# Performance work log

Measured on AMD Instinct MI355X. Metric: run time of the kernel, lower is better.

Reference implementation:

```python
import jax, jax.numpy as jnp
import numpy as np

N = 50000
E = 800000
IN_DIM = 256
HID = 32
HEADS = 4
OUT_DIM = 40
NEG_SLOPE = 0.2


def gat_layer(x, src, dst, W, a_src, a_dst, b, n_nodes, heads, ch, concat):
    # x: [N, F_in], W: [F_in, heads*ch], a_src/a_dst: [heads, ch], b: [out]
    h = (x @ W).reshape(n_nodes, heads, ch)                 # [N,H,C]
    alpha_s = jnp.einsum('nhc,hc->nh', h, a_src)            # [N,H]
    alpha_d = jnp.einsum('nhc,hc->nh', h, a_dst)            # [N,H]
    e = jax.nn.leaky_relu(alpha_s[src] + alpha_d[dst], NEG_SLOPE)  # [E,H]
    # segment softmax over destination neighborhoods (self-loops guarantee nonempty)
    m = jax.ops.segment_max(e, dst, num_segments=n_nodes)   # [N,H]
    e = jnp.exp(e - m[dst])
    denom = jax.ops.segment_sum(e, dst, num_segments=n_nodes)
    alpha = e / (denom[dst] + 1e-16)                         # [E,H]
    msg = h[src] * alpha[:, :, None]                         # [E,H,C]
    out = jax.ops.segment_sum(msg, dst, num_segments=n_nodes)  # [N,H,C]
    out = out.reshape(n_nodes, heads * ch) if concat else out.mean(axis=1)
    return out + b


def setup_inputs() -> dict:
    key = jax.random.key(0)
    ks = jax.random.split(key, 10)
    x = jax.random.normal(ks[0], (N, IN_DIM), dtype=jnp.float32)
    edge_index = jax.random.randint(ks[1], (2, E), 0, N, dtype=jnp.int32)
    s1 = 1.0 / np.sqrt(IN_DIM)
    s2 = 1.0 / np.sqrt(HID * HEADS)
    return {
        'x': x,
        'edge_index': edge_index,
        'W1': jax.random.normal(ks[2], (IN_DIM, HEADS * HID), dtype=jnp.float32) * s1,
        'a_src1': jax.random.normal(ks[3], (HEADS, HID), dtype=jnp.float32) * s1,
        'a_dst1': jax.random.normal(ks[4], (HEADS, HID), dtype=jnp.float32) * s1,
        'b1': jnp.zeros((HEADS * HID,), dtype=jnp.float32),
        'W2': jax.random.normal(ks[5], (HEADS * HID, OUT_DIM), dtype=jnp.float32) * s2,
        'a_src2': jax.random.normal(ks[6], (1, OUT_DIM), dtype=jnp.float32) * s2,
        'a_dst2': jax.random.normal(ks[7], (1, OUT_DIM), dtype=jnp.float32) * s2,
        'b2': jnp.zeros((OUT_DIM,), dtype=jnp.float32),
    }


def reference(x, edge_index, W1, a_src1, a_dst1, b1, W2, a_src2, a_dst2, b2):
    # PyG GATConv adds self-loops by default
    loops = jnp.arange(N, dtype=edge_index.dtype)
    src = jnp.concatenate([edge_index[0], loops])
    dst = jnp.concatenate([edge_index[1], loops])
    h = gat_layer(x, src, dst, W1, a_src1, a_dst1, b1, N, HEADS, HID, True)
    h = jax.nn.relu(h)
    out = gat_layer(h, src, dst, W2, a_src2, a_dst2, b2, N, 1, OUT_DIM, False)
    return jax.nn.log_softmax(out, axis=1)
```

## Files before the change

### kernel.cpp

```cpp
#include <hip/hip_runtime.h>
#include <math.h>

#define N_NODES 50000
#define N_EDGES 800000
#define IN_DIM  256
#define F1      128
#define HEADS   4
#define OUT_DIM 40
#define NEG     0.2f

#define NB   391
#define CAP  3072
#define EB   4096
#define PREW 16
#define G1B  782

typedef __attribute__((ext_vector_type(8))) short short8;
typedef __attribute__((ext_vector_type(4))) float float4v;

__device__ __forceinline__ unsigned short f2bf(float f) {
  unsigned int u = __float_as_uint(f);
  u += 0x7FFF + ((u >> 16) & 1);
  return (unsigned short)(u >> 16);
}
__device__ __forceinline__ float bf2f(unsigned short h) {
  return __uint_as_float((unsigned int)h << 16);
}
__device__ __forceinline__ float bflo(unsigned int u) { return __uint_as_float(u << 16); }
__device__ __forceinline__ float bfhi(unsigned int u) { return __uint_as_float(u & 0xffff0000u); }

__device__ __forceinline__ float lrelu(float e) { return e > 0.f ? e : e * NEG; }

__device__ __forceinline__ void gload_lds16(const void* g, void* l) {
  __builtin_amdgcn_global_load_lds(
      (const __attribute__((address_space(1))) unsigned int*)g,
      (__attribute__((address_space(3))) unsigned int*)l, 16, 0, 0);
}

__global__ __launch_bounds__(256) void pre_kernel(const float* __restrict__ W1,
                                                  unsigned short* __restrict__ wHi,
                                                  unsigned short* __restrict__ wLo,
                                                  const int* __restrict__ ei,
                                                  int* __restrict__ gcnt,
                                                  int2* __restrict__ gbucket) {
  __shared__ int smem[EB * 2 + NB * 3];
  if (blockIdx.x < PREW) {
    int tid = blockIdx.x * 256 + threadIdx.x;
    int kk = tid >> 9;
    int rest = tid & 511;
    int t = rest >> 6;
    int lane = rest & 63;
    int q = lane >> 4;
    int ln = lane & 15;
    int n = t * 16 + ln;
    unsigned int hi[4], lo[4];
#pragma unroll
    for (int jj = 0; jj < 4; jj++) {
      unsigned short h0, h1, l0, l1;
      {
        float v = W1[(kk * 32 + q * 8 + jj * 2) * F1 + n];
        h0 = f2bf(v); l0 = f2bf(v - bf2f(h0));
      }
      {
        float v = W1[(kk * 32 + q * 8 + jj * 2 + 1) * F1 + n];
        h1 = f2bf(v); l1 = f2bf(v - bf2f(h1));
      }
      hi[jj] = (unsigned int)h0 | ((unsigned int)h1 << 16);
      lo[jj] = (unsigned int)l0 | ((unsigned int)l1 << 16);
    }
    size_t base = (size_t)tid * 8;
    *(uint4*)&wHi[base] = make_uint4(hi[0], hi[1], hi[2], hi[3]);
    *(uint4*)&wLo[base] = make_uint4(lo[0], lo[1], lo[2], lo[3]);
  } else {
    int* ls = smem;
    int* ld = smem + EB;
    int* lcnt = smem + 2 * EB;
    int* lcur = lcnt + NB;
    int* gbaseS = lcur + NB;
    int tid = threadIdx.x;
    size_t base = (size_t)(blockIdx.x - PREW) * EB;
    for (int t = tid; t < NB; t += 256) { lcnt[t] = 0; lcur[t] = 0; }
    __syncthreads();
#pragma unroll
    for (int l = 0; l < EB / 256; l++) {
      int li = l * 256 + tid;
      size_t idx = base + li;
      int s = 0, d = -1;
      if (idx < N_EDGES) {
        s = ei[idx];
        d = ei[N_EDGES + idx];
        atomicAdd(&lcnt[d >> 7], 1);
      }
      ls[li] = s;
      ld[li] = d;
    }
    __syncthreads();
    for (int t = tid; t < NB; t += 256) gbaseS[t] = atomicAdd(&gcnt[t], lcnt[t]);
    __syncthreads();
#pragma unroll
    for (int l = 0; l < EB / 256; l++) {
      int li = l * 256 + tid;
      int d = ld[li];
      if (d >= 0) {
        int b = d >> 7;
        int r = gbaseS[b] + atomicAdd(&lcur[b], 1);
        if (r >= CAP) r = CAP - 1;
        gbucket[(size_t)b * CAP + r] = make_int2(ls[li], d);
      }
    }
  }
}

__global__ __launch_bounds__(256) void mid_kernel(
    const float* __restrict__ x, const unsigned short* __restrict__ wHi,
    const unsigned short* __restrict__ wLo,
    const float* __restrict__ a_src, const float* __restrict__ a_dst,
    unsigned short* __restrict__ h1b, float* __restrict__ as1, float* __restrict__ ad1,
    const int2* __restrict__ gbucket, const int* __restrict__ gcnt,
    int* __restrict__ row_ptr, int* __restrict__ col) {
  __shared__ short8 smem[2048];
  if (blockIdx.x < G1B) {
    short8 (*Bsh)[1024] = (short8(*)[1024])smem;
    int bid = blockIdx.x;
    int tid = threadIdx.x;
    int w = tid >> 6;
    int lane = tid & 63;
    int q = lane >> 4;
    int ln = lane & 15;
    int rowBase = bid * 64 + w * 16;
    int rowA = rowBase + ln;
    int rowAc = rowA < N_NODES ? rowA : N_NODES - 1;
    float4v acc[8];
#pragma unroll
    for (int t = 0; t < 8; t++) acc[t] = (float4v){0.f, 0.f, 0.f, 0.f};
    const short8* bhp = (const short8*)wHi;
    const short8* blp = (const short8*)wLo;

    auto prefetch = [&](int kk, int buf) {
#pragma unroll
      for (int c = 0; c < 2; c++) {
        int chunk = w * 2 + c;
        gload_lds16(bhp + (size_t)kk * 512 + chunk * 64 + lane, &Bsh[buf][chunk * 64]);
        gload_lds16(blp + (size_t)kk * 512 + chunk * 64 + lane, &Bsh[buf][512 + chunk * 64]);
      }
    };

    const float4* xbase = (const float4*)(x + (size_t)rowAc * IN_DIM + q * 8);
    float4 a0 = xbase[0];
    float4 a1 = xbase[1];
    prefetch(0, 0);
    __syncthreads();

#pragma unroll 1
    for (int kk = 0; kk < 8; kk++) {
      int buf = kk & 1;
      if (kk < 7) prefetch(kk + 1, buf ^ 1);
      int kn = (kk < 7) ? kk + 1 : 7;
      float4 n0 = xbase[kn * 8];
      float4 n1 = xbase[kn * 8 + 1];
      float av[8] = {a0.x, a0.y, a0.z, a0.w, a1.x, a1.y, a1.z, a1.w};
      short8 ahi, alo;
#pragma unroll
      for (int j = 0; j < 8; j++) {
        unsigned short hh = f2bf(av[j]);
        ahi[j] = (short)hh;
        alo[j] = (short)f2bf(av[j] - bf2f(hh));
      }
      const short8* bs = &Bsh[buf][0];
#pragma unroll
      for (int t = 0; t < 8; t++) {
        short8 bh = bs[t * 64 + lane];
        short8 bl = bs[512 + t * 64 + lane];
        acc[t] = __builtin_amdgcn_mfma_f32_16x16x32_bf16(ahi, bh, acc[t], 0, 0, 0);
        acc[t] = __builtin_amdgcn_mfma_f32_16x16x32_bf16(ahi, bl, acc[t], 0, 0, 0);
        acc[t] = __builtin_amdgcn_mfma_f32_16x16x32_bf16(alo, bh, acc[t], 0, 0, 0);
      }
      a0 = n0;
      a1 = n1;
      if (kk < 7) __syncthreads();
    }

    float asv[8], adv[8];
#pragma unroll
    for (int t = 0; t < 8; t++) {
      asv[t] = a_src[t * 16 + ln];
      adv[t] = a_dst[t * 16 + ln];
    }
#pragma unroll
    for (int reg = 0; reg < 4; reg++) {
      int r = rowBase + q * 4 + reg;
      bool valid = (r < N_NODES);
      if (valid) {
#pragma unroll
        for (int t = 0; t < 8; t++)
          h1b[(size_t)r * F1 + t * 16 + ln] = f2bf(acc[t][reg]);
      }
#pragma unroll
      for (int h = 0; h < 4; h++) {
        float sa = acc[2 * h][reg] * asv[2 * h] + acc[2 * h + 1][reg] * asv[2 * h + 1];
        float sd = acc[2 * h][reg] * adv[2 * h] + acc[2 * h + 1][reg] * adv[2 * h + 1];
#pragma unroll
        for (int off = 1; off < 16; off <<= 1) {
          sa += __shfl_xor(sa, off);
          sd += __shfl_xor(sd, off);
        }
        if (ln == 0 && valid) {
          as1[r * 4 + h] = sa;
          ad1[r * 4 + h] = sd;
        }
      }
    }
  } else {
    int2* ent = (int2*)smem;
    int* hcnt = (int*)(ent + CAP);
    int* sc   = hcnt + 128;
    int* cur  = sc + 128;
    int* red  = cur + 128;
    int b = blockIdx.x - G1B;
    int tid = threadIdx.x;
    int cnt = gcnt[b]; if (cnt > CAP) cnt = CAP;
    if (tid < 128) hcnt[tid] = 0;
    int part = 0;
    for (int i = tid; i < b; i += 256) part += gcnt[i];
#pragma unroll
    for (int off = 32; off > 0; off >>= 1) part += __shfl_xor(part, off);
    if ((tid & 63) == 0) red[tid >> 6] = part;
    __syncthreads();
    int base = red[0] + red[1] + red[2] + red[3];
    for (int i = tid; i < cnt; i += 256) {
      int2 e = gbucket[(size_t)b * CAP + i];
      ent[i] = e;
      atomicAdd(&hcnt[e.y & 127], 1);
    }
    __syncthreads();
    if (tid < 128) sc[tid] = hcnt[tid];
    __syncthreads();
    for (int off = 1; off < 128; off <<= 1) {
      int t = 0;
      if (tid < 128 && tid >= off) t = sc[tid - off];
      __syncthreads();
      if (tid < 128) sc[tid] += t;
      __syncthreads();
    }
    if (tid < 128) {
      int excl = sc[tid] - hcnt[tid];
      cur[tid] = excl;
      int node = (b << 7) + tid;
      if (node < N_NODES) row_ptr[node] = base + excl;
    }
    if (b == 0 && tid == 0) row_ptr[N_NODES] = N_EDGES;
    __syncthreads();
    for (int i = tid; i < cnt; i += 256) {
      int2 e = ent[i];
      int r = atomicAdd(&cur[e.y & 127], 1);
      col[base + r] = e.x;
    }
  }
}

__global__ __launch_bounds__(256) void gather1_kernel(
    const unsigned short* __restrict__ h1b, const float* __restrict__ as1,
    const float* __restrict__ ad1, const float* __restrict__ b1,
    const int* __restrict__ row_ptr, const int* __restrict__ col,
    float* __restrict__ x2) {
  int wv = threadIdx.x >> 6;
  int n = blockIdx.x * 4 + wv;
  if (n >= N_NODES) return;
  int lane = threadIdx.x & 63;
  int start = row_ptr[n];
  int deg = row_ptr[n + 1] - start;
  int slot = lane >> 4;
  int lane16 = lane & 15;
  int head = lane16 >> 2;
  float adh = ad1[n * 4 + head];
  float4 accA = make_float4(0.f, 0.f, 0.f, 0.f);
  float4 accB = make_float4(0.f, 0.f, 0.f, 0.f);
  float dn = 0.f;
  int i = slot;
  for (; i + 12 <= deg; i += 16) {
    int sA = col[start + i];
    int sB = col[start + i + 4];
    int sC = col[start + i + 8];
    int sD = (i + 12 < deg) ? col[start + i + 12] : n;
    float eA = __expf(lrelu(as1[sA * 4 + head] + adh));
    float eB = __expf(lrelu(as1[sB * 4 + head] + adh));
    float eC = __expf(lrelu(as1[sC * 4 + head] + adh));
    float eD = __expf(lrelu(as1[sD * 4 + head] + adh));
    uint4 uA = *(const uint4*)(h1b + (size_t)sA * F1 + lane16 * 8);
    uint4 uB = *(const uint4*)(h1b + (size_t)sB * F1 + lane16 * 8);
    uint4 uC = *(const uint4*)(h1b + (size_t)sC * F1 + lane16 * 8);
    uint4 uD = *(const uint4*)(h1b + (size_t)sD * F1 + lane16 * 8);
    dn += (eA + eB) + (eC + eD);
    accA.x += eA * bflo(uA.x); accA.y += eA * bfhi(uA.x);
    accA.z += eA * bflo(uA.y); accA.w += eA * bfhi(uA.y);
    accB.x += eA * bflo(uA.z); accB.y += eA * bfhi(uA.z);
    accB.z += eA * bflo(uA.w); accB.w += eA * bfhi(uA.w);
    accA.x += eB * bflo(uB.x); accA.y += eB * bfhi(uB.x);
    accA.z += eB * bflo(uB.y); accA.w += eB * bfhi(uB.y);
    accB.x += eB * bflo(uB.z); accB.y += eB * bfhi(uB.z);
    accB.z += eB * bflo(uB.w); accB.w += eB * bfhi(uB.w);
    accA.x += eC * bflo(uC.x); accA.y += eC * bfhi(uC.x);
    accA.z += eC * bflo(uC.y); accA.w += eC * bfhi(uC.y);
    accB.x += eC * bflo(uC.z); accB.y += eC * bfhi(uC.z);
    accB.z += eC * bflo(uC.w); accB.w += eC * bfhi(uC.w);
    accA.x += eD * bflo(uD.x); accA.y += eD * bfhi(uD.x);
    accA.z += eD * bflo(uD.y); accA.w += eD * bfhi(uD.y);
    accB.x += eD * bflo(uD.z); accB.y += eD * bfhi(uD.z);
    accB.z += eD * bflo(uD.w); accB.w += eD * bfhi(uD.w);
  }
  for (; i + 4 <= deg; i += 8) {
    int sA = col[start + i];
    int sB = (i + 4 < deg) ? col[start + i + 4] : n;
    float eA = __expf(lrelu(as1[sA * 4 + head] + adh));
    float eB = __expf(lrelu(as1[sB * 4 + head] + adh));
    uint4 uA = *(const uint4*)(h1b + (size_t)sA * F1 + lane16 * 8);
    uint4 uB = *(const uint4*)(h1b + (size_t)sB * F1 + lane16 * 8);
    dn += eA + eB;
    accA.x += eA * bflo(uA.x); accA.y += eA * bfhi(uA.x);
    accA.z += eA * bflo(uA.y); accA.w += eA * bfhi(uA.y);
    accB.x += eA * bflo(uA.z); accB.y += eA * bfhi(uA.z);
    accB.z += eA * bflo(uA.w); accB.w += eA * bfhi(uA.w);
    accA.x += eB * bflo(uB.x); accA.y += eB * bfhi(uB.x);
    accA.z += eB * bflo(uB.y); accA.w += eB * bfhi(uB.y);
    accB.x += eB * bflo(uB.z); accB.y += eB * bfhi(uB.z);
    accB.z += eB * bflo(uB.w); accB.w += eB * bfhi(uB.w);
  }
  if (i <= deg) {
    int s = (i < deg) ? col[start + i] : n;
    float e = __expf(lrelu(as1[s * 4 + head] + adh));
    uint4 u = *(const uint4*)(h1b + (size_t)s * F1 + lane16 * 8);
    dn += e;
    accA.x += e * bflo(u.x); accA.y += e * bfhi(u.x);
    accA.z += e * bflo(u.y); accA.w += e * bfhi(u.y);
    accB.x += e * bflo(u.z); accB.y += e * bfhi(u.z);
    accB.z += e * bflo(u.w); accB.w += e * bfhi(u.w);
  }
#pragma unroll
  for (int off = 16; off <= 32; off <<= 1) {
    accA.x += __shfl_xor(accA.x, off); accA.y += __shfl_xor(accA.y, off);
    accA.z += __shfl_xor(accA.z, off); accA.w += __shfl_xor(accA.w, off);
    accB.x += __shfl_xor(accB.x, off); accB.y += __shfl_xor(accB.y, off);
    accB.z += __shfl_xor(accB.z, off); accB.w += __shfl_xor(accB.w, off);
    dn += __shfl_xor(dn, off);
  }
  if (slot == 0) {
    float rsh = 1.f / (dn + 1e-16f);
    float4 bA = *(const float4*)&b1[lane16 * 8];
    float4 bB = *(const float4*)&b1[lane16 * 8 + 4];
    float4 oA, oB;
    oA.x = fmaxf(accA.x * rsh + bA.x, 0.f); oA.y = fmaxf(accA.y * rsh + bA.y, 0.f);
    oA.z = fmaxf(accA.z * rsh + bA.z, 0.f); oA.w = fmaxf(accA.w * rsh + bA.w, 0.f);
    oB.x = fmaxf(accB.x * rsh + bB.x, 0.f); oB.y = fmaxf(accB.y * rsh + bB.y, 0.f);
    oB.z = fmaxf(accB.z * rsh + bB.z, 0.f); oB.w = fmaxf(accB.w * rsh + bB.w, 0.f);
    *(float4*)&x2[(size_t)n * F1 + lane16 * 8] = oA;
    *(float4*)&x2[(size_t)n * F1 + lane16 * 8 + 4] = oB;
  }
}

__global__ __launch_bounds__(256) void gemm2_kernel(
    const float* __restrict__ x2, const float* __restrict__ W2,
    const float* __restrict__ asv, const float* __restrict__ adv,
    unsigned short* __restrict__ h2b, float* __restrict__ as2, float* __restrict__ ad2) {
  __shared__ float xs[64][132];
  __shared__ float W2s[128][44];
  __shared__ float asv_s[40], adv_s[40];
  int tid = threadIdx.x;
  int bm = blockIdx.x * 64;
#pragma unroll
  for (int l = 0; l < 8; l++) {
    int idx = tid + l * 256;
    int r = idx >> 5;
    int c4 = (idx & 31) << 2;
    float4 v = make_float4(0.f, 0.f, 0.f, 0.f);
    if (bm + r < N_NODES) v = *(const float4*)&x2[(size_t)(bm + r) * F1 + c4];
    *(float4*)&xs[r][c4] = v;
  }
#pragma unroll
  for (int l = 0; l < 5; l++) {
    int idx = tid + l * 256;
    int k = idx / 10;
    int c4 = (idx - k * 10) * 4;
    *(float4*)&W2s[k][c4] = *(const float4*)&W2[k * OUT_DIM + c4];
  }
  if (tid < OUT_DIM) { asv_s[tid] = asv[tid]; adv_s[tid] = adv[tid]; }
  __syncthreads();
  int r = tid >> 2;
  int cb = (tid & 3) * 10;
  float acc[10] = {0.f};
  for (int k = 0; k < F1; k++) {
    float xv = xs[r][k];
#pragma unroll
    for (int c = 0; c < 10; c++) acc[c] += xv * W2s[k][cb + c];
  }
  int grow = bm + r;
  float sa = 0.f, sd = 0.f;
#pragma unroll
  for (int c = 0; c < 10; c++) {
    sa += acc[c] * asv_s[cb + c];
    sd += acc[c] * adv_s[cb + c];
  }
#pragma unroll
  for (int off = 1; off < 4; off <<= 1) {
    sa += __shfl_xor(sa, off);
    sd += __shfl_xor(sd, off);
  }
  if (grow < N_NODES) {
#pragma unroll
    for (int c = 0; c < 10; c += 2) {
      unsigned int p = ((unsigned int)f2bf(acc[c + 1]) << 16) | f2bf(acc[c]);
      *(unsigned int*)&h2b[(size_t)grow * OUT_DIM + cb + c] = p;
    }
    if ((tid & 3) == 0) { as2[grow] = sa; ad2[grow] = sd; }
  }
}

__global__ __launch_bounds__(256) void gather2_kernel(
    const unsigned short* __restrict__ h2b, const float* __restrict__ as2,
    const float* __restrict__ ad2, const float* __restrict__ b2,
    const int* __restrict__ row_ptr, const int* __restrict__ col,
    float* __restrict__ out) {
  int wv = threadIdx.x >> 6;
  int n = blockIdx.x * 4 + wv;
  if (n >= N_NODES) return;
  int lane = threadIdx.x & 63;
  int start = row_ptr[n];
  int deg = row_ptr[n + 1] - start;
  float adh = ad2[n];
  int slot = lane / 5;
  int c = lane - slot * 5;
  float4 accA = make_float4(0.f, 0.f, 0.f, 0.f);
  float4 accB = make_float4(0.f, 0.f, 0.f, 0.f);
  float dn = 0.f;
  if (slot < 12) {
    int i = slot;
    for (; i + 12 <= deg; i += 24) {
      int sA = col[start + i];
      int sB = (i + 12 < deg) ? col[start + i + 12] : n;
      float eA = __expf(lrelu(as2[sA] + adh));
      float eB = __expf(lrelu(as2[sB] + adh));
      uint4 uA = *(const uint4*)(h2b + (size_t)sA * OUT_DIM + c * 8);
      uint4 uB = *(const uint4*)(h2b + (size_t)sB * OUT_DIM + c * 8);
      dn += eA + eB;
      accA.x += eA * bflo(uA.x); accA.y += eA * bfhi(uA.x);
      accA.z += eA * bflo(uA.y); accA.w += eA * bfhi(uA.y);
      accB.x += eA * bflo(uA.z); accB.y += eA * bfhi(uA.z);
      accB.z += eA * bflo(uA.w); accB.w += eA * bfhi(uA.w);
      accA.x += eB * bflo(uB.x); accA.y += eB * bfhi(uB.x);
      accA.z += eB * bflo(uB.y); accA.w += eB * bfhi(uB.y);
      accB.x += eB * bflo(uB.z); accB.y += eB * bfhi(uB.z);
      accB.z += eB * bflo(uB.w); accB.w += eB * bfhi(uB.w);
    }
    if (i <= deg) {
      int src = (i < deg) ? col[start + i] : n;
      float e = __expf(lrelu(as2[src] + adh));
      uint4 u = *(const uint4*)(h2b + (size_t)src * OUT_DIM + c * 8);
      dn += e;
      accA.x += e * bflo(u.x); accA.y += e * bfhi(u.x);
      accA.z += e * bflo(u.y); accA.w += e * bfhi(u.y);
      accB.x += e * bflo(u.z); accB.y += e * bfhi(u.z);
      accB.z += e * bflo(u.w); accB.w += e * bfhi(u.w);
    }
  }
  float v[9] = {accA.x, accA.y, accA.z, accA.w, accB.x, accB.y, accB.z, accB.w, dn};
#pragma unroll
  for (int k = 0; k < 9; k++) v[k] += __shfl(v[k], lane + 30);
#pragma unroll
  for (int k = 0; k < 9; k++) v[k] += __shfl(v[k], lane + 15);
  {
    float t1[9], t2[9];
#pragma unroll
    for (int k = 0; k < 9; k++) t1[k] = __shfl(v[k], lane + 5);
#pragma unroll
    for (int k = 0; k < 9; k++) t2[k] = __shfl(v[k], lane + 10);
#pragma unroll
    for (int k = 0; k < 9; k++) v[k] += t1[k] + t2[k];
  }
  bool owner = (slot == 0);
  float vals[8];
  float lmax = -1e30f, lsum = 0.f;
  if (owner) {
    float rs = 1.f / (v[8] + 1e-16f);
#pragma unroll
    for (int k = 0; k < 8; k++) {
      vals[k] = v[k] * rs + b2[c * 8 + k];
      lmax = fmaxf(lmax, vals[k]);
    }
  }
  float gmax = lmax;
#pragma unroll
  for (int off = 32; off > 0; off >>= 1) gmax = fmaxf(gmax, __shfl_xor(gmax, off));
  if (owner) {
#pragma unroll
    for (int k = 0; k < 8; k++) lsum += __expf(vals[k] - gmax);
  }
#pragma unroll
  for (int off = 32; off > 0; off >>= 1) lsum += __shfl_xor(lsum, off);
  if (owner) {
    float lse = gmax + __logf(lsum);
    float4 oA = make_float4(vals[0] - lse, vals[1] - lse, vals[2] - lse, vals[3] - lse);
    float4 oB = make_float4(vals[4] - lse, vals[5] - lse, vals[6] - lse, vals[7] - lse);
    *(float4*)&out[(size_t)n * OUT_DIM + c * 8] = oA;
    *(float4*)&out[(size_t)n * OUT_DIM + c * 8 + 4] = oB;
  }
}

extern "C" void kernel_launch(void* const* d_in, const int* in_sizes, int n_in,
                              void* d_out, int out_size, void* d_ws, size_t ws_size,
                              hipStream_t stream) {
  const float* x      = (const float*)d_in[0];
  const int*   ei     = (const int*)d_in[1];
  const float* W1     = (const float*)d_in[2];
  const float* a_src1 = (const float*)d_in[3];
  const float* a_dst1 = (const float*)d_in[4];
  const float* b1     = (const float*)d_in[5];
  const float* W2     = (const float*)d_in[6];
  const float* a_src2 = (const float*)d_in[7];
  const float* a_dst2 = (const float*)d_in[8];
  const float* b2     = (const float*)d_in[9];
  float* out = (float*)d_out;

  char* ws = (char*)d_ws;
  size_t off = 0;
  auto alloc = [&](size_t bytes) -> void* {
    void* p = ws + off;
    off += (bytes + 255) & ~(size_t)255;
    return p;
  };
  unsigned short* h1b = (unsigned short*)alloc((size_t)N_NODES * F1 * 2);
  unsigned short* h2b = (unsigned short*)alloc((size_t)N_NODES * OUT_DIM * 2);
  unsigned short* wHi = (unsigned short*)alloc((size_t)IN_DIM * F1 * 2);
  unsigned short* wLo = (unsigned short*)alloc((size_t)IN_DIM * F1 * 2);
  float* as1    = (float*)alloc((size_t)N_NODES * HEADS * 4);
  float* ad1    = (float*)alloc((size_t)N_NODES * HEADS * 4);
  float* x2     = (float*)alloc((size_t)N_NODES * F1 * 4);
  float* as2    = (float*)alloc((size_t)N_NODES * 4);
  float* ad2    = (float*)alloc((size_t)N_NODES * 4);
  int* row_ptr  = (int*)alloc((size_t)(N_NODES + 1) * 4);
  int* col      = (int*)alloc((size_t)N_EDGES * 4);
  int* gcnt     = (int*)alloc((size_t)NB * 4);
  int2* gbucket = (int2*)alloc((size_t)NB * CAP * 8);

  hipMemsetAsync(gcnt, 0, (size_t)NB * 4, stream);
  pre_kernel<<<PREW + (N_EDGES + EB - 1) / EB, 256, 0, stream>>>(W1, wHi, wLo, ei, gcnt, gbucket);
  mid_kernel<<<G1B + NB, 256, 0, stream>>>(x, wHi, wLo, a_src1, a_dst1, h1b, as1, ad1,
                                           gbucket, gcnt, row_ptr, col);
  gather1_kernel<<<(N_NODES + 3) / 4, 256, 0, stream>>>(h1b, as1, ad1, b1, row_ptr, col, x2);

  gemm2_kernel<<<(N_NODES + 63) / 64, 256, 0, stream>>>(x2, W2, a_src2, a_dst2, h2b, as2, ad2);
  gather2_kernel<<<(N_NODES + 3) / 4, 256, 0, stream>>>(h2b, as2, ad2, b2, row_ptr, col, out);
}
```

Measured before the change: 233.4 us.

## Run second-layer GEMM on bf16 MFMA with hi/lo split precision

Replaces the scalar FP32 LDS-tiled gemm2 with MFMA 16x16x32 bf16 instructions, using a three-term hi/lo split to keep near-FP32 accuracy. gather1 now writes x2 as separate bf16 hi and lo arrays, and pre_kernel gains extra blocks that pre-split W2 into an MFMA-friendly padded layout. The goal is to cut the scalar FMA and LDS cost of gemm2. In exchange it adds conversion work in gather1, triples the MFMA count, and does scattered 2-byte h2b stores.

```diff
diff --git a/kernel.cpp b/kernel.cpp
--- a/kernel.cpp
+++ b/kernel.cpp
@@ -7,12 +7,14 @@
 #define F1      128
 #define HEADS   4
 #define OUT_DIM 40
+#define N2PAD   48
 #define NEG     0.2f
 
 #define NB   391
 #define CAP  3072
 #define EB   4096
 #define PREW 16
+#define W2PB 3
 #define G1B  782
 
 typedef __attribute__((ext_vector_type(8))) short short8;
@@ -40,6 +42,9 @@
 __global__ __launch_bounds__(256) void pre_kernel(const float* __restrict__ W1,
                                                   unsigned short* __restrict__ wHi,
                                                   unsigned short* __restrict__ wLo,
+                                                  const float* __restrict__ W2,
+                                                  unsigned short* __restrict__ w2h,
+                                                  unsigned short* __restrict__ w2l,
                                                   const int* __restrict__ ei,
                                                   int* __restrict__ gcnt,
                                                   int2* __restrict__ gbucket) {
@@ -71,6 +76,35 @@
     size_t base = (size_t)tid * 8;
     *(uint4*)&wHi[base] = make_uint4(hi[0], hi[1], hi[2], hi[3]);
     *(uint4*)&wLo[base] = make_uint4(lo[0], lo[1], lo[2], lo[3]);
+  } else if (blockIdx.x < PREW + W2PB) {
+    int fid = (blockIdx.x - PREW) * 256 + threadIdx.x;
+    if (fid < 768) {
+      int kk = fid / 192;
+      int rest = fid - kk * 192;
+      int t = rest >> 6;
+      int lane = rest & 63;
+      int q = lane >> 4;
+      int ln = lane & 15;
+      int n = t * 16 + ln;
+      unsigned int hi[4], lo[4];
+#pragma unroll
+      for (int jj = 0; jj < 4; jj++) {
+        unsigned short h0, h1, l0, l1;
+        {
+          float v = (n < OUT_DIM) ? W2[(kk * 32 + q * 8 + jj * 2) * OUT_DIM + n] : 0.f;
+          h0 = f2bf(v); l0 = f2bf(v - bf2f(h0));
+        }
+        {
+          float v = (n < OUT_DIM) ? W2[(kk * 32 + q * 8 + jj * 2 + 1) * OUT_DIM + n] : 0.f;
+          h1 = f2bf(v); l1 = f2bf(v - bf2f(h1));
+        }
+        hi[jj] = (unsigned int)h0 | ((unsigned int)h1 << 16);
+        lo[jj] = (unsigned int)l0 | ((unsigned int)l1 << 16);
+      }
+      size_t base = (size_t)fid * 8;
+      *(uint4*)&w2h[base] = make_uint4(hi[0], hi[1], hi[2], hi[3]);
+      *(uint4*)&w2l[base] = make_uint4(lo[0], lo[1], lo[2], lo[3]);
+    }
   } else {
     int* ls = smem;
     int* ld = smem + EB;
@@ -78,7 +112,7 @@
     int* lcur = lcnt + NB;
     int* gbaseS = lcur + NB;
     int tid = threadIdx.x;
-    size_t base = (size_t)(blockIdx.x - PREW) * EB;
+    size_t base = (size_t)(blockIdx.x - PREW - W2PB) * EB;
     for (int t = tid; t < NB; t += 256) { lcnt[t] = 0; lcur[t] = 0; }
     __syncthreads();
 #pragma unroll
@@ -262,7 +296,7 @@
     const unsigned short* __restrict__ h1b, const float* __restrict__ as1,
     const float* __restrict__ ad1, const float* __restrict__ b1,
     const int* __restrict__ row_ptr, const int* __restrict__ col,
-    float* __restrict__ x2) {
+    unsigned short* __restrict__ x2h, unsigned short* __restrict__ x2l) {
   int wv = threadIdx.x >> 6;
   int n = blockIdx.x * 4 + wv;
   if (n >= N_NODES) return;
@@ -347,70 +381,85 @@
     float rsh = 1.f / (dn + 1e-16f);
     float4 bA = *(const float4*)&b1[lane16 * 8];
     float4 bB = *(const float4*)&b1[lane16 * 8 + 4];
-    float4 oA, oB;
-    oA.x = fmaxf(accA.x * rsh + bA.x, 0.f); oA.y = fmaxf(accA.y * rsh + bA.y, 0.f);
-    oA.z = fmaxf(accA.z * rsh + bA.z, 0.f); oA.w = fmaxf(accA.w * rsh + bA.w, 0.f);
-    oB.x = fmaxf(accB.x * rsh + bB.x, 0.f); oB.y = fmaxf(accB.y * rsh + bB.y, 0.f);
-    oB.z = fmaxf(accB.z * rsh + bB.z, 0.f); oB.w = fmaxf(accB.w * rsh + bB.w, 0.f);
-    *(float4*)&x2[(size_t)n * F1 + lane16 * 8] = oA;
-    *(float4*)&x2[(size_t)n * F1 + lane16 * 8 + 4] = oB;
+    float o[8];
+    o[0] = fmaxf(accA.x * rsh + bA.x, 0.f); o[1] = fmaxf(accA.y * rsh + bA.y, 0.f);
+    o[2] = fmaxf(accA.z * rsh + bA.z, 0.f); o[3] = fmaxf(accA.w * rsh + bA.w, 0.f);
+    o[4] = fmaxf(accB.x * rsh + bB.x, 0.f); o[5] = fmaxf(accB.y * rsh + bB.y, 0.f);
+    o[6] = fmaxf(accB.z * rsh + bB.z, 0.f); o[7] = fmaxf(accB.w * rsh + bB.w, 0.f);
+    unsigned int hw[4], lw[4];
+#pragma unroll
+    for (int p = 0; p < 4; p++) {
+      unsigned short h0 = f2bf(o[2 * p]);
+      unsigned short h1 = f2bf(o[2 * p + 1]);
+      unsigned short l0 = f2bf(o[2 * p] - bf2f(h0));
+      unsigned short l1 = f2bf(o[2 * p + 1] - bf2f(h1));
+      hw[p] = (unsigned int)h0 | ((unsigned int)h1 << 16);
+      lw[p] = (unsigned int)l0 | ((unsigned int)l1 << 16);
+    }
+    *(uint4*)&x2h[(size_t)n * F1 + lane16 * 8] = make_uint4(hw[0], hw[1], hw[2], hw[3]);
+    *(uint4*)&x2l[(size_t)n * F1 + lane16 * 8] = make_uint4(lw[0], lw[1], lw[2], lw[3]);
   }
 }
 
 __global__ __launch_bounds__(256) void gemm2_kernel(
-    const float* __restrict__ x2, const float* __restrict__ W2,
-    const float* __restrict__ asv, const float* __restrict__ adv,
+    const unsigned short* __restrict__ x2h, const unsigned short* __restrict__ x2l,
+    const unsigned short* __restrict__ w2h, const unsigned short* __restrict__ w2l,
+    const float* __restrict__ a2s, const float* __restrict__ a2d,
     unsigned short* __restrict__ h2b, float* __restrict__ as2, float* __restrict__ ad2) {
-  __shared__ float xs[64][132];
-  __shared__ float W2s[128][44];
-  __shared__ float asv_s[40], adv_s[40];
   int tid = threadIdx.x;
-  int bm = blockIdx.x * 64;
-#pragma unroll
-  for (int l = 0; l < 8; l++) {
-    int idx = tid + l * 256;
-    int r = idx >> 5;
-    int c4 = (idx & 31) << 2;
-    float4 v = make_float4(0.f, 0.f, 0.f, 0.f);
-    if (bm + r < N_NODES) v = *(const float4*)&x2[(size_t)(bm + r) * F1 + c4];
-    *(float4*)&xs[r][c4] = v;
-  }
-#pragma unroll
-  for (int l = 0; l < 5; l++) {
-    int idx = tid + l * 256;
-    int k = idx / 10;
-    int c4 = (idx - k * 10) * 4;
-    *(float4*)&W2s[k][c4] = *(const float4*)&W2[k * OUT_DIM + c4];
-  }
-  if (tid < OUT_DIM) { asv_s[tid] = asv[tid]; adv_s[tid] = adv[tid]; }
-  __syncthreads();
-  int r = tid >> 2;
-  int cb = (tid & 3) * 10;
-  float acc[10] = {0.f};
-  for (int k = 0; k < F1; k++) {
-    float xv = xs[r][k];
-#pragma unroll
-    for (int c = 0; c < 10; c++) acc[c] += xv * W2s[k][cb + c];
-  }
-  int grow = bm + r;
-  float sa = 0.f, sd = 0.f;
-#pragma unroll
-  for (int c = 0; c < 10; c++) {
-    sa += acc[c] * asv_s[cb + c];
-    sd += acc[c] * adv_s[cb + c];
-  }
-#pragma unroll
-  for (int off = 1; off < 4; off <<= 1) {
-    sa += __shfl_xor(sa, off);
-    sd += __shfl_xor(sd, off);
-  }
-  if (grow < N_NODES) {
-#pragma unroll
-    for (int c = 0; c < 10; c += 2) {
-      unsigned int p = ((unsigned int)f2bf(acc[c + 1]) << 16) | f2bf(acc[c]);
-      *(unsigned int*)&h2b[(size_t)grow * OUT_DIM + cb + c] = p;
-    }
-    if ((tid & 3) == 0) { as2[grow] = sa; ad2[grow] = sd; }
+  int w = tid >> 6;
+  int lane = tid & 63;
+  int q = lane >> 4;
+  int ln = lane & 15;
+  int rowBase = blockIdx.x * 64 + w * 16;
+  int rowA = rowBase + ln;
+  int rowAc = rowA < N_NODES ? rowA : N_NODES - 1;
+  float4v acc[3];
+#pragma unroll
+  for (int t = 0; t < 3; t++) acc[t] = (float4v){0.f, 0.f, 0.f, 0.f};
+  const short8* ahp = (const short8*)(x2h + (size_t)rowAc * F1);
+  const short8* alp = (const short8*)(x2l + (size_t)rowAc * F1);
+  const short8* bhp = (const short8*)w2h;
+  const short8* blp = (const short8*)w2l;
+#pragma unroll
+  for (int kk = 0; kk < 4; kk++) {
+    short8 ahi = ahp[kk * 4 + q];
+    short8 alo = alp[kk * 4 + q];
+#pragma unroll
+    for (int t = 0; t < 3; t++) {
+      short8 bh = bhp[(kk * 3 + t) * 64 + lane];
+      short8 bl = blp[(kk * 3 + t) * 64 + lane];
+      acc[t] = __builtin_amdgcn_mfma_f32_16x16x32_bf16(ahi, bh, acc[t], 0, 0, 0);
+      acc[t] = __builtin_amdgcn_mfma_f32_16x16x32_bf16(ahi, bl, acc[t], 0, 0, 0);
+      acc[t] = __builtin_amdgcn_mfma_f32_16x16x32_bf16(alo, bh, acc[t], 0, 0, 0);
+    }
+  }
+  float a2sv[3], a2dv[3];
+#pragma unroll
+  for (int t = 0; t < 3; t++) {
+    int n = t * 16 + ln;
+    a2sv[t] = (n < OUT_DIM) ? a2s[n] : 0.f;
+    a2dv[t] = (n < OUT_DIM) ? a2d[n] : 0.f;
+  }
+#pragma unroll
+  for (int reg = 0; reg < 4; reg++) {
+    int r = rowBase + q * 4 + reg;
+    bool valid = (r < N_NODES);
+    float sa = acc[0][reg] * a2sv[0] + acc[1][reg] * a2sv[1] + acc[2][reg] * a2sv[2];
+    float sd = acc[0][reg] * a2dv[0] + acc[1][reg] * a2dv[1] + acc[2][reg] * a2dv[2];
+#pragma unroll
+    for (int off = 1; off < 16; off <<= 1) {
+      sa += __shfl_xor(sa, off);
+      sd += __shfl_xor(sd, off);
+    }
+    if (valid) {
+#pragma unroll
+      for (int t = 0; t < 3; t++) {
+        int n = t * 16 + ln;
+        if (n < OUT_DIM) h2b[(size_t)r * OUT_DIM + n] = f2bf(acc[t][reg]);
+      }
+      if (ln == 0) { as2[r] = sa; ad2[r] = sd; }
+    }
   }
 }
 
@@ -530,9 +579,12 @@
   unsigned short* h2b = (unsigned short*)alloc((size_t)N_NODES * OUT_DIM * 2);
   unsigned short* wHi = (unsigned short*)alloc((size_t)IN_DIM * F1 * 2);
   unsigned short* wLo = (unsigned short*)alloc((size_t)IN_DIM * F1 * 2);
+  unsigned short* w2h = (unsigned short*)alloc((size_t)768 * 8 * 2);
+  unsigned short* w2l = (unsigned short*)alloc((size_t)768 * 8 * 2);
   float* as1    = (float*)alloc((size_t)N_NODES * HEADS * 4);
   float* ad1    = (float*)alloc((size_t)N_NODES * HEADS * 4);
-  float* x2     = (float*)alloc((size_t)N_NODES * F1 * 4);
+  unsigned short* x2h = (unsigned short*)alloc((size_t)N_NODES * F1 * 2);
+  unsigned short* x2l = (unsigned short*)alloc((size_t)N_NODES * F1 * 2);
   float* as2    = (float*)alloc((size_t)N_NODES * 4);
   float* ad2    = (float*)alloc((size_t)N_NODES * 4);
   int* row_ptr  = (int*)alloc((size_t)(N_NODES + 1) * 4);
@@ -541,11 +593,13 @@
   int2* gbucket = (int2*)alloc((size_t)NB * CAP * 8);
 
   hipMemsetAsync(gcnt, 0, (size_t)NB * 4, stream);
-  pre_kernel<<<PREW + (N_EDGES + EB - 1) / EB, 256, 0, stream>>>(W1, wHi, wLo, ei, gcnt, gbucket);
+  pre_kernel<<<PREW + W2PB + (N_EDGES + EB - 1) / EB, 256, 0, stream>>>(
+      W1, wHi, wLo, W2, w2h, w2l, ei, gcnt, gbucket);
   mid_kernel<<<G1B + NB, 256, 0, stream>>>(x, wHi, wLo, a_src1, a_dst1, h1b, as1, ad1,
                                            gbucket, gcnt, row_ptr, col);
-  gather1_kernel<<<(N_NODES + 3) / 4, 256, 0, stream>>>(h1b, as1, ad1, b1, row_ptr, col, x2);
-
-  gemm2_kernel<<<(N_NODES + 63) / 64, 256, 0, stream>>>(x2, W2, a_src2, a_dst2, h2b, as2, ad2);
+  gather1_kernel<<<(N_NODES + 3) / 4, 256, 0, stream>>>(h1b, as1, ad1, b1, row_ptr, col,
+                                                        x2h, x2l);
+  gemm2_kernel<<<(N_NODES + 63) / 64, 256, 0, stream>>>(x2h, x2l, w2h, w2l,
+                                                        a_src2, a_dst2, h2b, as2, ad2);
   gather2_kernel<<<(N_NODES + 3) / 4, 256, 0, stream>>>(h2b, as2, ad2, b2, row_ptr, col, out);
 }
```

Result: faster. 216.9 us, median of 2 (-7.0%).
